# Kernel optimization log

Hardware: AMD Instinct MI355X
Metric: run time of the kernel (lower is better)

## Reference

```python
import jax, jax.numpy as jnp
import numpy as np

N_NODES = 65536   # sli * node = 512 * 128
N_EDGES = 524288  # avg degree 8
SLI, NODE = 512, 128
SLOPE = 0.01      # nn.LeakyReLU default negative_slope


def leaky_relu(v):
    return jnp.where(v >= 0, v, SLOPE * v)


def graph_conv(h, src, dst, W, b):
    """DGL GraphConv with norm='both': D_in^{-1/2} A D_out^{-1/2} h W + b, then LeakyReLU."""
    ones = jnp.ones(src.shape[0], dtype=h.dtype)
    out_deg = jnp.clip(jax.ops.segment_sum(ones, src, num_segments=N_NODES), 1.0)
    in_deg = jnp.clip(jax.ops.segment_sum(ones, dst, num_segments=N_NODES), 1.0)
    h = h * jax.lax.rsqrt(out_deg)[:, None]                     # src-side norm
    agg = jax.ops.segment_sum(h[src], dst, num_segments=N_NODES)  # gather + scatter-add
    agg = agg * jax.lax.rsqrt(in_deg)[:, None]                  # dst-side norm
    return leaky_relu(agg @ W + b)


def graphsage(x, src, dst, W, b):
    # x: [sli, C, node] -> [sli*node, C] -> GraphConv -> [sli, F, node]
    sli, C, node = x.shape
    h = x.transpose(0, 2, 1).reshape(-1, C)
    h = graph_conv(h, src, dst, W, b)
    return h.reshape(sli, node, -1).transpose(0, 2, 1)


def conv1x1(x, W, b):
    # pointwise Conv1d: x [S, Cin, N], W [Cout, Cin] -> [S, Cout, N]
    return jnp.einsum('scn,oc->son', x, W) + b[None, :, None]


def setup_inputs() -> dict:
    key = jax.random.key(0)
    ks = jax.random.split(key, 16)
    d = {
        'x': jax.random.normal(ks[0], (SLI, 128, NODE), dtype=jnp.float32),
        'edge_src': jax.random.randint(ks[1], (N_EDGES,), 0, N_NODES, dtype=jnp.int32),
        'edge_dst': jax.random.randint(ks[2], (N_EDGES,), 0, N_NODES, dtype=jnp.int32),
        'W_head': jax.random.normal(ks[3], (128, 128), dtype=jnp.float32) * 0.05,
        'b_head': jnp.zeros((128,), dtype=jnp.float32),
        'W_res0': jax.random.normal(ks[4], (128, 128), dtype=jnp.float32) * 0.05,
        'b_res0': jnp.zeros((128,), dtype=jnp.float32),
        'W_res1': jax.random.normal(ks[5], (128, 128), dtype=jnp.float32) * 0.05,
        'b_res1': jnp.zeros((128,), dtype=jnp.float32),
        'W_res2': jax.random.normal(ks[6], (128, 128), dtype=jnp.float32) * 0.05,
        'b_res2': jnp.zeros((128,), dtype=jnp.float32),
        'W_fusion': jax.random.normal(ks[7], (256, 512), dtype=jnp.float32) * 0.05,
        'b_fusion': jnp.zeros((256,), dtype=jnp.float32),
        'W_p1': jax.random.normal(ks[8], (256, 768), dtype=jnp.float32) * 0.05,
        'b_p1': jnp.zeros((256,), dtype=jnp.float32),
        'W_p2': jax.random.normal(ks[9], (64, 256), dtype=jnp.float32) * 0.05,
        'b_p2': jnp.zeros((64,), dtype=jnp.float32),
        'W_p3': jax.random.normal(ks[10], (2, 64), dtype=jnp.float32) * 0.05,
        'b_p3': jnp.zeros((2,), dtype=jnp.float32),
    }
    return d


def reference(x, edge_src, edge_dst, W_head, b_head, W_res0, b_res0, W_res1, b_res1,
              W_res2, b_res2, W_fusion, b_fusion, W_p1, b_p1, W_p2, b_p2, W_p3, b_p3):
    h = graphsage(x, edge_src, edge_dst, W_head, b_head)   # [S, 128, N]
    states = [h]
    for W, b in ((W_res0, b_res0), (W_res1, b_res1), (W_res2, b_res2)):
        h = graphsage(h, edge_src, edge_dst, W, b) + h     # residual
        states.append(h)
    state = jnp.concatenate(states, axis=1)                # [S, 512, N]
    fused = conv1x1(state, W_fusion, b_fusion)             # [S, 256, N]
    global_state = jnp.max(fused, axis=2, keepdims=True)   # [S, 256, 1]
    global_state = jnp.broadcast_to(global_state, (state.shape[0], 256, state.shape[2]))
    state = jnp.concatenate([global_state, state], axis=1) # [S, 768, N]
    y = leaky_relu(conv1x1(state, W_p1, b_p1))
    y = leaky_relu(conv1x1(y, W_p2, b_p2))
    return conv1x1(y, W_p3, b_p3)                          # [S, 2, N]
```

## Files before the change

kernel.cpp:

```cpp
#include <hip/hip_runtime.h>

#define NN 65536
#define NE 524288
#define SLOPE 0.01f

typedef unsigned short us;
typedef __attribute__((ext_vector_type(8))) short short8;
typedef __attribute__((ext_vector_type(4))) float f32x4;

__device__ __forceinline__ float leaky(float v) { return v >= 0.f ? v : SLOPE * v; }
__device__ __forceinline__ float b2f(us u) { return __uint_as_float(((unsigned)u) << 16); }
__device__ __forceinline__ us f2b(float f) {
  unsigned u = __float_as_uint(f);
  u += 0x7fffu + ((u >> 16) & 1u);
  return (us)(u >> 16);
}
__device__ __forceinline__ void split2(float v, us& hi, us& lo) {
  hi = f2b(v);
  lo = f2b(v - b2f(hi));
}

__device__ __forceinline__ void gload16(const void* g, void* l) {
  __builtin_amdgcn_global_load_lds(
      (const __attribute__((address_space(1))) unsigned int*)g,
      (__attribute__((address_space(3))) unsigned int*)l, 16, 0, 0);
}

__global__ void zero_ints(int* __restrict__ p, int n) {
  int i = blockIdx.x * blockDim.x + threadIdx.x;
  if (i < n) p[i] = 0;
}

__global__ void deg_count(const int* __restrict__ src, const int* __restrict__ dst,
                          int* __restrict__ cout, int* __restrict__ cin) {
  int e = blockIdx.x * blockDim.x + threadIdx.x;
  if (e < NE) {
    atomicAdd(&cout[src[e]], 1);
    atomicAdd(&cin[dst[e]], 1);
  }
}

__global__ void rs_kernel(const int* __restrict__ cout, const int* __restrict__ cin,
                          float* __restrict__ rs_out, float* __restrict__ rs_in) {
  int n = blockIdx.x * blockDim.x + threadIdx.x;
  if (n < NN) {
    rs_out[n] = rsqrtf((float)(cout[n] > 0 ? cout[n] : 1));
    rs_in[n]  = rsqrtf((float)(cin[n]  > 0 ? cin[n]  : 1));
  }
}

__global__ __launch_bounds__(1024) void scan_kernel(const int* __restrict__ cnt,
                                                    int* __restrict__ row_ptr) {
  __shared__ int part[1024];
  int t = threadIdx.x;
  int base = t * 64;
  int s = 0;
  for (int i = 0; i < 64; ++i) s += cnt[base + i];
  part[t] = s;
  __syncthreads();
  for (int d = 1; d < 1024; d <<= 1) {
    int v = (t >= d) ? part[t - d] : 0;
    __syncthreads();
    part[t] += v;
    __syncthreads();
  }
  int run = part[t] - s;
  for (int i = 0; i < 64; ++i) { row_ptr[base + i] = run; run += cnt[base + i]; }
  if (t == 1023) row_ptr[NN] = run;
}

__global__ void csr_fill(const int* __restrict__ src, const int* __restrict__ dst,
                         const int* __restrict__ row_ptr, int* __restrict__ cursor,
                         int* __restrict__ csr) {
  int e = blockIdx.x * blockDim.x + threadIdx.x;
  if (e < NE) {
    int d = dst[e];
    int pos = atomicAdd(&cursor[d], 1);
    csr[row_ptr[d] + pos] = src[e];
  }
}

__global__ __launch_bounds__(256) void transpose_x(const float* __restrict__ x,
                                                   us* __restrict__ h0h,
                                                   us* __restrict__ h0l) {
  __shared__ float tile[128][68];
  int s  = blockIdx.x >> 1;
  int vh = (blockIdx.x & 1) * 64;
  const float* xs = x + (size_t)s * 16384;
  int t = threadIdx.x;
  int v4 = t & 15, c0 = t >> 4;
  for (int p = 0; p < 8; ++p) {
    int c = c0 + p * 16;
    float4 val = *(const float4*)(xs + (size_t)c * 128 + vh + v4 * 4);
    *(float4*)&tile[c][v4 * 4] = val;
  }
  __syncthreads();
  int c4 = t & 31, v0 = t >> 5;
  for (int p = 0; p < 8; ++p) {
    int v = v0 + p * 8;
    float o[4];
    o[0] = tile[c4 * 4 + 0][v];
    o[1] = tile[c4 * 4 + 1][v];
    o[2] = tile[c4 * 4 + 2][v];
    o[3] = tile[c4 * 4 + 3][v];
    us hh[4], ll[4];
#pragma unroll
    for (int j = 0; j < 4; ++j) split2(o[j], hh[j], ll[j]);
    size_t off = (size_t)(s * 128 + vh + v) * 128 + c4 * 4;
    uint2 wh = make_uint2((unsigned)hh[0] | ((unsigned)hh[1] << 16),
                          (unsigned)hh[2] | ((unsigned)hh[3] << 16));
    uint2 wl = make_uint2((unsigned)ll[0] | ((unsigned)ll[1] << 16),
                          (unsigned)ll[2] | ((unsigned)ll[3] << 16));
    *(uint2*)(h0h + off) = wh;
    *(uint2*)(h0l + off) = wl;
  }
}

__global__ void wsplit(const float* __restrict__ src, us* __restrict__ bh,
                       us* __restrict__ bl, int N, int K, int ld, int koff) {
  int idx = blockIdx.x * 256 + threadIdx.x;
  if (idx >= N * K) return;
  int n = idx / K, k = idx - n * K;
  float v = src[(size_t)n * ld + koff + k];
  us hi, lo; split2(v, hi, lo);
  bh[idx] = hi; bl[idx] = lo;
}

__global__ void wsplit_t(const float* __restrict__ src, us* __restrict__ bh,
                         us* __restrict__ bl, int N, int K, int ld) {
  int idx = blockIdx.x * 256 + threadIdx.x;
  if (idx >= N * K) return;
  int n = idx / K, k = idx - n * K;
  float v = src[(size_t)k * ld + n];
  us hi, lo; split2(v, hi, lo);
  bh[idx] = hi; bl[idx] = lo;
}

__global__ __launch_bounds__(256) void aggregate(
    const us* __restrict__ hh, const us* __restrict__ hl, int lda,
    const int* __restrict__ row_ptr, const int* __restrict__ csr,
    const float* __restrict__ rs_out, const float* __restrict__ rs_in,
    us* __restrict__ aggh, us* __restrict__ aggl) {
  const int lane = threadIdx.x & 63;
  const int n = blockIdx.x * 4 + (threadIdx.x >> 6);
  const us* base = ((lane < 32) ? hh : hl) + (size_t)(lane & 31) * 4;
  const int b = row_ptr[n], e = row_ptr[n + 1];
  float a0 = 0.f, a1 = 0.f, a2 = 0.f, a3 = 0.f;
  int i = b;
  for (; i + 4 <= e; i += 4) {
    int s0 = csr[i], s1 = csr[i + 1], s2 = csr[i + 2], s3 = csr[i + 3];
    uint2 v0 = *(const uint2*)(base + (size_t)s0 * lda);
    uint2 v1 = *(const uint2*)(base + (size_t)s1 * lda);
    uint2 v2 = *(const uint2*)(base + (size_t)s2 * lda);
    uint2 v3 = *(const uint2*)(base + (size_t)s3 * lda);
    float w0 = rs_out[s0], w1 = rs_out[s1], w2 = rs_out[s2], w3 = rs_out[s3];
    a0 = fmaf(w0, __uint_as_float(v0.x << 16), a0);
    a1 = fmaf(w0, __uint_as_float(v0.x & 0xffff0000u), a1);
    a2 = fmaf(w0, __uint_as_float(v0.y << 16), a2);
    a3 = fmaf(w0, __uint_as_float(v0.y & 0xffff0000u), a3);
    a0 = fmaf(w1, __uint_as_float(v1.x << 16), a0);
    a1 = fmaf(w1, __uint_as_float(v1.x & 0xffff0000u), a1);
    a2 = fmaf(w1, __uint_as_float(v1.y << 16), a2);
    a3 = fmaf(w1, __uint_as_float(v1.y & 0xffff0000u), a3);
    a0 = fmaf(w2, __uint_as_float(v2.x << 16), a0);
    a1 = fmaf(w2, __uint_as_float(v2.x & 0xffff0000u), a1);
    a2 = fmaf(w2, __uint_as_float(v2.y << 16), a2);
    a3 = fmaf(w2, __uint_as_float(v2.y & 0xffff0000u), a3);
    a0 = fmaf(w3, __uint_as_float(v3.x << 16), a0);
    a1 = fmaf(w3, __uint_as_float(v3.x & 0xffff0000u), a1);
    a2 = fmaf(w3, __uint_as_float(v3.y << 16), a2);
    a3 = fmaf(w3, __uint_as_float(v3.y & 0xffff0000u), a3);
  }
  for (; i < e; ++i) {
    int s0 = csr[i];
    uint2 v0 = *(const uint2*)(base + (size_t)s0 * lda);
    float w0 = rs_out[s0];
    a0 = fmaf(w0, __uint_as_float(v0.x << 16), a0);
    a1 = fmaf(w0, __uint_as_float(v0.x & 0xffff0000u), a1);
    a2 = fmaf(w0, __uint_as_float(v0.y << 16), a2);
    a3 = fmaf(w0, __uint_as_float(v0.y & 0xffff0000u), a3);
  }
  a0 += __shfl_xor(a0, 32);
  a1 += __shfl_xor(a1, 32);
  a2 += __shfl_xor(a2, 32);
  a3 += __shfl_xor(a3, 32);
  const float ri = rs_in[n];
  a0 *= ri; a1 *= ri; a2 *= ri; a3 *= ri;
  us h[4], l[4];
  split2(a0, h[0], l[0]); split2(a1, h[1], l[1]);
  split2(a2, h[2], l[2]); split2(a3, h[3], l[3]);
  size_t o = (size_t)n * 128 + (size_t)(lane & 31) * 4;
  if (lane < 32) {
    uint2 wv = make_uint2((unsigned)h[0] | ((unsigned)h[1] << 16),
                          (unsigned)h[2] | ((unsigned)h[3] << 16));
    *(uint2*)(aggh + o) = wv;
  } else {
    uint2 wv = make_uint2((unsigned)l[0] | ((unsigned)l[1] << 16),
                          (unsigned)l[2] | ((unsigned)l[3] << 16));
    *(uint2*)(aggl + o) = wv;
  }
}

template<int KTOT, int NF, int MODE, int NSPLIT>
__global__ __launch_bounds__(512, 4) void mgemm(
    const us* __restrict__ Ah, const us* __restrict__ Al, int lda,
    const us* __restrict__ Bh, const us* __restrict__ Bl,
    const float* __restrict__ bias,
    float* __restrict__ outf, us* __restrict__ outh, us* __restrict__ outl,
    int ldo, int colOff,
    const us* __restrict__ prevh, const us* __restrict__ prevl,
    const float* __restrict__ gcon) {
  constexpr int BN  = NF * 64;
  constexpr int LB  = (NF == 2) ? 7 : 6;
  constexpr int NT  = KTOT / 32;
  constexpr int LPT = 2 + (BN * 8) / 512;

  __shared__ __align__(16) us sAh[2][4][128][8];
  __shared__ __align__(16) us sAl[2][4][128][8];
  __shared__ __align__(16) us sBh[2][4][BN][8];
  __shared__ __align__(16) us sBl[2][4][BN][8];

  const int t = threadIdx.x;
  int mb, nb;
  if constexpr (NSPLIT == 2) {
    int lid = (blockIdx.x & 7) * ((int)gridDim.x >> 3) + (blockIdx.x >> 3);
    mb = lid >> 1; nb = lid & 1;
  } else {
    mb = blockIdx.x; nb = 0;
  }
  const int mbase = mb * 128;
  const int nbase = nb * BN;

  const us* gp[LPT];
  us* lp0[LPT];
  us* lp1[LPT];
#pragma unroll
  for (int i = 0; i < LPT; ++i) {
    int id = i * 512 + t;
    if (id < 512) {
      int row = id & 127, kb = id >> 7;
      gp[i]  = Ah + (size_t)(mbase + row) * lda + kb * 8;
      lp0[i] = &sAh[0][kb][row][0];
      lp1[i] = &sAh[1][kb][row][0];
    } else if (id < 1024) {
      int c = id - 512;
      int row = c & 127, kb = c >> 7;
      gp[i]  = Al + (size_t)(mbase + row) * lda + kb * 8;
      lp0[i] = &sAl[0][kb][row][0];
      lp1[i] = &sAl[1][kb][row][0];
    } else if (id < 1024 + BN * 4) {
      int c = id - 1024;
      int row = c & (BN - 1), kb = c >> LB;
      gp[i]  = Bh + (size_t)(nbase + row) * KTOT + kb * 8;
      lp0[i] = &sBh[0][kb][row][0];
      lp1[i] = &sBh[1][kb][row][0];
    } else {
      int c = id - 1024 - BN * 4;
      int row = c & (BN - 1), kb = c >> LB;
      gp[i]  = Bl + (size_t)(nbase + row) * KTOT + kb * 8;
      lp0[i] = &sBl[0][kb][row][0];
      lp1[i] = &sBl[1][kb][row][0];
    }
  }

  const int lane = t & 63, wvi = t >> 6;
  const int wm = wvi & 1, wn = wvi >> 1;
  const int l15 = lane & 15, lkb = lane >> 4;

  f32x4 acc[4][NF];
#pragma unroll
  for (int i = 0; i < 4; ++i)
#pragma unroll
    for (int j = 0; j < NF; ++j)
#pragma unroll
      for (int e = 0; e < 4; ++e) acc[i][j][e] = 0.f;

  auto stageb = [&](us* const* lp, int k0) {
#pragma unroll
    for (int i = 0; i < LPT; ++i) gload16(gp[i] + k0, lp[i]);
  };
  auto waitL = [&]() {
    if constexpr (LPT == 4) asm volatile("s_waitcnt vmcnt(4)" ::: "memory");
    else                    asm volatile("s_waitcnt vmcnt(3)" ::: "memory");
    __builtin_amdgcn_sched_barrier(0);
  };
  auto wait0 = [&]() {
    asm volatile("s_waitcnt vmcnt(0)" ::: "memory");
    __builtin_amdgcn_sched_barrier(0);
  };
  auto bar = [&]() {
    __builtin_amdgcn_s_barrier();
    __builtin_amdgcn_sched_barrier(0);
  };
  auto kstep = [&](us (&bAh)[4][128][8], us (&bAl)[4][128][8],
                   us (&bBh)[4][BN][8], us (&bBl)[4][BN][8]) {
    short8 ah[4], al[4], bh[NF], bl[NF];
#pragma unroll
    for (int fm = 0; fm < 4; ++fm) {
      ah[fm] = *(const short8*)&bAh[lkb][wm * 64 + fm * 16 + l15][0];
      al[fm] = *(const short8*)&bAl[lkb][wm * 64 + fm * 16 + l15][0];
    }
#pragma unroll
    for (int fn = 0; fn < NF; ++fn) {
      bh[fn] = *(const short8*)&bBh[lkb][wn * (NF * 16) + fn * 16 + l15][0];
      bl[fn] = *(const short8*)&bBl[lkb][wn * (NF * 16) + fn * 16 + l15][0];
    }
    __builtin_amdgcn_s_setprio(1);
#pragma unroll
    for (int fm = 0; fm < 4; ++fm)
#pragma unroll
      for (int fn = 0; fn < NF; ++fn)
        acc[fm][fn] = __builtin_amdgcn_mfma_f32_16x16x32_bf16(ah[fm], bh[fn], acc[fm][fn], 0, 0, 0);
#pragma unroll
    for (int fm = 0; fm < 4; ++fm)
#pragma unroll
      for (int fn = 0; fn < NF; ++fn)
        acc[fm][fn] = __builtin_amdgcn_mfma_f32_16x16x32_bf16(al[fm], bh[fn], acc[fm][fn], 0, 0, 0);
#pragma unroll
    for (int fm = 0; fm < 4; ++fm)
#pragma unroll
      for (int fn = 0; fn < NF; ++fn)
        acc[fm][fn] = __builtin_amdgcn_mfma_f32_16x16x32_bf16(ah[fm], bl[fn], acc[fm][fn], 0, 0, 0);
    __builtin_amdgcn_s_setprio(0);
  };

  stageb(lp0, 0);
  stageb(lp1, 32);
#pragma unroll 1
  for (int kt = 0; kt < NT; kt += 2) {
    waitL(); bar();
    kstep(sAh[0], sAl[0], sBh[0], sBl[0]);
    bar();
    if (kt + 2 < NT) stageb(lp0, (kt + 2) * 32);
    if (kt + 3 < NT) waitL(); else wait0();
    bar();
    kstep(sAh[1], sAl[1], sBh[1], sBl[1]);
    bar();
    if (kt + 3 < NT) stageb(lp1, (kt + 3) * 32);
  }

  if constexpr (MODE == 0 || MODE == 1 || MODE == 3) {
    const float* gc = (MODE == 3) ? (gcon + (size_t)mb * 256 + nbase) : nullptr;
#pragma unroll
    for (int fm = 0; fm < 4; ++fm)
#pragma unroll
      for (int fn = 0; fn < NF; ++fn) {
        const int col = wn * (NF * 16) + fn * 16 + l15;
        float bb = bias[nbase + col];
        if constexpr (MODE == 3) bb += gc[col];
#pragma unroll
        for (int r = 0; r < 4; ++r) {
          const int row = mbase + wm * 64 + fm * 16 + lkb * 4 + r;
          float v = leaky(acc[fm][fn][r] + bb);
          const size_t off = (size_t)row * ldo + colOff + nbase + col;
          if constexpr (MODE == 1) v += b2f(prevh[off - 128]) + b2f(prevl[off - 128]);
          us hi, lo; split2(v, hi, lo);
          outh[off] = hi;
          outl[off] = lo;
        }
      }
  } else if constexpr (MODE == 2) {
    __shared__ float red[2][128];
#pragma unroll
    for (int fn = 0; fn < NF; ++fn) {
      float m = acc[0][fn][0];
#pragma unroll
      for (int fm = 0; fm < 4; ++fm)
#pragma unroll
        for (int r = 0; r < 4; ++r) m = fmaxf(m, acc[fm][fn][r]);
      m = fmaxf(m, __shfl_xor(m, 16));
      m = fmaxf(m, __shfl_xor(m, 32));
      if (lane < 16) red[wm][wn * (NF * 16) + fn * 16 + l15] = m;
    }
    __syncthreads();
    if (t < 128)
      outf[(size_t)mb * 256 + nbase + t] = fmaxf(red[0][t], red[1][t]) + bias[nbase + t];
  } else {
#pragma unroll
    for (int fm = 0; fm < 4; ++fm) {
      const int col = wn * 16 + l15;
      const float bb = bias[col];
#pragma unroll
      for (int r = 0; r < 4; ++r) {
        const int row = mbase + wm * 64 + fm * 16 + lkb * 4 + r;
        outf[(size_t)row * 64 + col] = leaky(acc[fm][0][r] + bb);
      }
    }
  }
}

__global__ void gcon_kernel(const float* __restrict__ gmax, const float* __restrict__ Wp1,
                            float* __restrict__ gcon) {
  __shared__ float g[256];
  int s = blockIdx.x, o = threadIdx.x;
  g[o] = gmax[(size_t)s * 256 + o];
  __syncthreads();
  float acc = 0.f;
  const float* wr = Wp1 + (size_t)o * 768;
#pragma unroll 8
  for (int c = 0; c < 256; ++c) acc += g[c] * wr[c];
  gcon[(size_t)s * 256 + o] = acc;
}

__global__ void p3_kernel(const float* __restrict__ y2, const float* __restrict__ W,
                          const float* __restrict__ b, float* __restrict__ out) {
  __shared__ float w0[64], w1[64];
  int t = threadIdx.x;
  if (t < 64) { w0[t] = W[t]; w1[t] = W[64 + t]; }
  __syncthreads();
  int n = blockIdx.x * 256 + t;
  const float* row = y2 + (size_t)n * 64;
  float a0 = b[0], a1 = b[1];
#pragma unroll
  for (int j = 0; j < 64; j += 4) {
    float4 v = *(const float4*)(row + j);
    a0 += v.x * w0[j] + v.y * w0[j + 1] + v.z * w0[j + 2] + v.w * w0[j + 3];
    a1 += v.x * w1[j] + v.y * w1[j + 1] + v.z * w1[j + 2] + v.w * w1[j + 3];
  }
  int s = n >> 7, vv = n & 127;
  out[((size_t)s * 2 + 0) * 128 + vv] = a0;
  out[((size_t)s * 2 + 1) * 128 + vv] = a1;
}

extern "C" void kernel_launch(void* const* d_in, const int* in_sizes, int n_in,
                              void* d_out, int out_size, void* d_ws, size_t ws_size,
                              hipStream_t stream) {
  const float* x        = (const float*)d_in[0];
  const int*   esrc     = (const int*)d_in[1];
  const int*   edst     = (const int*)d_in[2];
  const float* W_head   = (const float*)d_in[3];
  const float* b_head   = (const float*)d_in[4];
  const float* W_res[3] = {(const float*)d_in[5], (const float*)d_in[7], (const float*)d_in[9]};
  const float* b_res[3] = {(const float*)d_in[6], (const float*)d_in[8], (const float*)d_in[10]};
  const float* W_fusion = (const float*)d_in[11];
  const float* b_fusion = (const float*)d_in[12];
  const float* W_p1     = (const float*)d_in[13];
  const float* b_p1     = (const float*)d_in[14];
  const float* W_p2     = (const float*)d_in[15];
  const float* b_p2     = (const float*)d_in[16];
  const float* W_p3     = (const float*)d_in[17];
  const float* b_p3     = (const float*)d_in[18];
  float* outp = (float*)d_out;

  char* w = (char*)d_ws;
  size_t off = 0;
  auto alloc = [&](size_t bytes) { char* p = w + off; off += (bytes + 255) & ~(size_t)255; return p; };

  us* states_h = (us*)alloc((size_t)NN * 512 * 2);
  us* states_l = (us*)alloc((size_t)NN * 512 * 2);
  char* regionA = alloc((size_t)NN * 128 * 2 * 4);
  us* h0h  = (us*)regionA;
  us* h0l  = (us*)(regionA + (size_t)NN * 128 * 2);
  us* aggh = (us*)(regionA + (size_t)NN * 128 * 4);
  us* aggl = (us*)(regionA + (size_t)NN * 128 * 6);
  us* y1h  = (us*)regionA;
  us* y1l  = (us*)(regionA + (size_t)NN * 256 * 2);
  float* y2 = (float*)states_h;

  float* gmax   = (float*)alloc(512 * 256 * 4);
  float* gcon   = (float*)alloc(512 * 256 * 4);
  float* rs_out = (float*)alloc((size_t)NN * 4);
  float* rs_in  = (float*)alloc((size_t)NN * 4);
  us* cWh[4]; us* cWl[4];
  for (int l = 0; l < 4; ++l) { cWh[l] = (us*)alloc(128 * 128 * 2); cWl[l] = (us*)alloc(128 * 128 * 2); }
  us* fWh  = (us*)alloc(256 * 512 * 2);
  us* fWl  = (us*)alloc(256 * 512 * 2);
  us* p1Wh = (us*)alloc(256 * 512 * 2);
  us* p1Wl = (us*)alloc(256 * 512 * 2);
  us* p2Wh = (us*)alloc(64 * 256 * 2);
  us* p2Wl = (us*)alloc(64 * 256 * 2);
  int* cnt_out = (int*)alloc((size_t)NN * 4);
  int* cnt_in  = (int*)alloc((size_t)NN * 4);
  int* cursor  = (int*)alloc((size_t)NN * 4);
  int* row_ptr = (int*)alloc(((size_t)NN + 1) * 4);
  int* csr     = (int*)alloc((size_t)NE * 4);

  zero_ints<<<(3 * NN + 255) / 256, 256, 0, stream>>>(cnt_out, 3 * NN);
  deg_count<<<NE / 256, 256, 0, stream>>>(esrc, edst, cnt_out, cnt_in);
  rs_kernel<<<NN / 256, 256, 0, stream>>>(cnt_out, cnt_in, rs_out, rs_in);
  scan_kernel<<<1, 1024, 0, stream>>>(cnt_in, row_ptr);
  csr_fill<<<NE / 256, 256, 0, stream>>>(esrc, edst, row_ptr, cursor, csr);

  transpose_x<<<1024, 256, 0, stream>>>(x, h0h, h0l);
  const float* cW[4] = {W_head, W_res[0], W_res[1], W_res[2]};
  for (int l = 0; l < 4; ++l)
    wsplit_t<<<64, 256, 0, stream>>>(cW[l], cWh[l], cWl[l], 128, 128, 128);
  wsplit<<<512, 256, 0, stream>>>(W_fusion, fWh, fWl, 256, 512, 512, 0);
  wsplit<<<512, 256, 0, stream>>>(W_p1, p1Wh, p1Wl, 256, 512, 768, 256);
  wsplit<<<64, 256, 0, stream>>>(W_p2, p2Wh, p2Wl, 64, 256, 256, 0);

  const float* cB[4] = {b_head, b_res[0], b_res[1], b_res[2]};
  aggregate<<<NN / 4, 256, 0, stream>>>(h0h, h0l, 128, row_ptr, csr, rs_out, rs_in, aggh, aggl);
  mgemm<128, 2, 0, 1><<<512, 512, 0, stream>>>(aggh, aggl, 128, cWh[0], cWl[0], cB[0],
                                               nullptr, states_h, states_l, 512, 0,
                                               nullptr, nullptr, nullptr);
  for (int l = 1; l <= 3; ++l) {
    aggregate<<<NN / 4, 256, 0, stream>>>(states_h + (size_t)(l - 1) * 128,
                                          states_l + (size_t)(l - 1) * 128, 512,
                                          row_ptr, csr, rs_out, rs_in, aggh, aggl);
    mgemm<128, 2, 1, 1><<<512, 512, 0, stream>>>(aggh, aggl, 128, cWh[l], cWl[l], cB[l],
                                                 nullptr, states_h, states_l, 512, l * 128,
                                                 states_h, states_l, nullptr);
  }
  mgemm<512, 2, 2, 2><<<1024, 512, 0, stream>>>(states_h, states_l, 512, fWh, fWl, b_fusion,
                                                gmax, nullptr, nullptr, 0, 0,
                                                nullptr, nullptr, nullptr);
  gcon_kernel<<<512, 256, 0, stream>>>(gmax, W_p1, gcon);
  mgemm<512, 2, 3, 2><<<1024, 512, 0, stream>>>(states_h, states_l, 512, p1Wh, p1Wl, b_p1,
                                                nullptr, y1h, y1l, 256, 0,
                                                nullptr, nullptr, gcon);
  mgemm<256, 1, 4, 1><<<512, 512, 0, stream>>>(y1h, y1l, 256, p2Wh, p2Wl, b_p2,
                                               y2, nullptr, nullptr, 0, 0,
                                               nullptr, nullptr, nullptr);
  p3_kernel<<<NN / 256, 256, 0, stream>>>(y2, W_p3, b_p3, outp);
}
```

Baseline: 628.4 us.

## Replace GEMM kernel with 256-row tiles covering full N per block

Rewrites the split-bf16 MFMA GEMM to process 256 rows per block and the full output width (up to 256 columns) in one block, with a flat LDS buffer and phased fragment loads separated by barriers. This removes the N-split and the cross-block max reduction, and reduces redundant reloading of A tiles across column blocks. In exchange, LDS use and register pressure per block grow and there are fewer blocks (256) than CUs on some launches, which may reduce occupancy and latency hiding.

```diff
diff --git a/kernel.cpp b/kernel.cpp
--- a/kernel.cpp
+++ b/kernel.cpp
@@ -201,8 +201,8 @@
   }
 }
 
-template<int KTOT, int NF, int MODE, int NSPLIT>
-__global__ __launch_bounds__(512, 4) void mgemm(
+template<int KTOT, int BN, int WM, int PH, int MODE>
+__global__ __launch_bounds__(512) void mgemm8(
     const us* __restrict__ Ah, const us* __restrict__ Al, int lda,
     const us* __restrict__ Bh, const us* __restrict__ Bl,
     const float* __restrict__ bias,
@@ -210,149 +210,134 @@
     int ldo, int colOff,
     const us* __restrict__ prevh, const us* __restrict__ prevl,
     const float* __restrict__ gcon) {
-  constexpr int BN  = NF * 64;
-  constexpr int LB  = (NF == 2) ? 7 : 6;
+  constexpr int WN  = 8 / WM;
+  constexpr int FM  = 16 / WM;
+  constexpr int FMP = FM / PH;
   constexpr int NT  = KTOT / 32;
-  constexpr int LPT = 2 + (BN * 8) / 512;
-
-  __shared__ __align__(16) us sAh[2][4][128][8];
-  __shared__ __align__(16) us sAl[2][4][128][8];
-  __shared__ __align__(16) us sBh[2][4][BN][8];
-  __shared__ __align__(16) us sBl[2][4][BN][8];
+  constexpr int LBN = (BN == 256) ? 8 : ((BN == 128) ? 7 : 6);
+  constexpr int CHT = 2048 + BN * 8;
+  constexpr int LPT = CHT / 512;
+
+  __shared__ __align__(16) us L[2][CHT * 8];
 
   const int t = threadIdx.x;
-  int mb, nb;
-  if constexpr (NSPLIT == 2) {
-    int lid = (blockIdx.x & 7) * ((int)gridDim.x >> 3) + (blockIdx.x >> 3);
-    mb = lid >> 1; nb = lid & 1;
-  } else {
-    mb = blockIdx.x; nb = 0;
-  }
-  const int mbase = mb * 128;
-  const int nbase = nb * BN;
+  const int mbase = blockIdx.x * 256;
 
   const us* gp[LPT];
-  us* lp0[LPT];
-  us* lp1[LPT];
 #pragma unroll
   for (int i = 0; i < LPT; ++i) {
     int id = i * 512 + t;
-    if (id < 512) {
-      int row = id & 127, kb = id >> 7;
-      gp[i]  = Ah + (size_t)(mbase + row) * lda + kb * 8;
-      lp0[i] = &sAh[0][kb][row][0];
-      lp1[i] = &sAh[1][kb][row][0];
-    } else if (id < 1024) {
-      int c = id - 512;
-      int row = c & 127, kb = c >> 7;
-      gp[i]  = Al + (size_t)(mbase + row) * lda + kb * 8;
-      lp0[i] = &sAl[0][kb][row][0];
-      lp1[i] = &sAl[1][kb][row][0];
-    } else if (id < 1024 + BN * 4) {
-      int c = id - 1024;
-      int row = c & (BN - 1), kb = c >> LB;
-      gp[i]  = Bh + (size_t)(nbase + row) * KTOT + kb * 8;
-      lp0[i] = &sBh[0][kb][row][0];
-      lp1[i] = &sBh[1][kb][row][0];
+    if (id < 1024) {
+      int row = id & 255, kb = id >> 8;
+      gp[i] = Ah + (size_t)(mbase + row) * lda + kb * 8;
+    } else if (id < 2048) {
+      int c = id - 1024, row = c & 255, kb = c >> 8;
+      gp[i] = Al + (size_t)(mbase + row) * lda + kb * 8;
+    } else if (id < 2048 + BN * 4) {
+      int c = id - 2048, row = c & (BN - 1), kb = c >> LBN;
+      gp[i] = Bh + (size_t)row * KTOT + kb * 8;
     } else {
-      int c = id - 1024 - BN * 4;
-      int row = c & (BN - 1), kb = c >> LB;
-      gp[i]  = Bl + (size_t)(nbase + row) * KTOT + kb * 8;
-      lp0[i] = &sBl[0][kb][row][0];
-      lp1[i] = &sBl[1][kb][row][0];
+      int c = id - 2048 - BN * 4, row = c & (BN - 1), kb = c >> LBN;
+      gp[i] = Bl + (size_t)row * KTOT + kb * 8;
     }
   }
 
   const int lane = t & 63, wvi = t >> 6;
-  const int wm = wvi & 1, wn = wvi >> 1;
+  const int wm = wvi & (WM - 1), wn = wvi / WM;
   const int l15 = lane & 15, lkb = lane >> 4;
-
-  f32x4 acc[4][NF];
-#pragma unroll
-  for (int i = 0; i < 4; ++i)
-#pragma unroll
-    for (int j = 0; j < NF; ++j)
+  const int wrow = wm * (256 / WM);
+
+  f32x4 acc[FM][4];
+#pragma unroll
+  for (int i = 0; i < FM; ++i)
+#pragma unroll
+    for (int j = 0; j < 4; ++j)
 #pragma unroll
       for (int e = 0; e < 4; ++e) acc[i][j][e] = 0.f;
 
-  auto stageb = [&](us* const* lp, int k0) {
-#pragma unroll
-    for (int i = 0; i < LPT; ++i) gload16(gp[i] + k0, lp[i]);
+  auto stage = [&](us* Lb, int k0) {
+#pragma unroll
+    for (int i = 0; i < LPT; ++i)
+      gload16(gp[i] + k0, Lb + (size_t)(i * 512 + t) * 8);
   };
   auto waitL = [&]() {
-    if constexpr (LPT == 4) asm volatile("s_waitcnt vmcnt(4)" ::: "memory");
-    else                    asm volatile("s_waitcnt vmcnt(3)" ::: "memory");
+    if constexpr (LPT == 8)      asm volatile("s_waitcnt vmcnt(8)" ::: "memory");
+    else if constexpr (LPT == 6) asm volatile("s_waitcnt vmcnt(6)" ::: "memory");
+    else                         asm volatile("s_waitcnt vmcnt(5)" ::: "memory");
     __builtin_amdgcn_sched_barrier(0);
   };
   auto wait0 = [&]() {
     asm volatile("s_waitcnt vmcnt(0)" ::: "memory");
     __builtin_amdgcn_sched_barrier(0);
   };
-  auto bar = [&]() {
-    __builtin_amdgcn_s_barrier();
-    __builtin_amdgcn_sched_barrier(0);
+  auto phases = [&](const us* Lb) {
+#pragma unroll
+    for (int p = 0; p < PH; ++p) {
+      short8 ah[FMP], al[FMP], bh[4], bl[4];
+#pragma unroll
+      for (int f = 0; f < FMP; ++f) {
+        const int arow = wrow + (p * FMP + f) * 16 + l15;
+        ah[f] = *(const short8*)(Lb + ((size_t)(lkb * 256 + arow)) * 8);
+        al[f] = *(const short8*)(Lb + ((size_t)(1024 + lkb * 256 + arow)) * 8);
+      }
+#pragma unroll
+      for (int fn = 0; fn < 4; ++fn) {
+        const int bcol = wn * 64 + fn * 16 + l15;
+        bh[fn] = *(const short8*)(Lb + ((size_t)(2048 + lkb * BN + bcol)) * 8);
+        bl[fn] = *(const short8*)(Lb + ((size_t)(2048 + BN * 4 + lkb * BN + bcol)) * 8);
+      }
+      __builtin_amdgcn_s_setprio(1);
+#pragma unroll
+      for (int f = 0; f < FMP; ++f)
+#pragma unroll
+        for (int fn = 0; fn < 4; ++fn)
+          acc[p * FMP + f][fn] =
+              __builtin_amdgcn_mfma_f32_16x16x32_bf16(ah[f], bh[fn], acc[p * FMP + f][fn], 0, 0, 0);
+#pragma unroll
+      for (int f = 0; f < FMP; ++f)
+#pragma unroll
+        for (int fn = 0; fn < 4; ++fn)
+          acc[p * FMP + f][fn] =
+              __builtin_amdgcn_mfma_f32_16x16x32_bf16(al[f], bh[fn], acc[p * FMP + f][fn], 0, 0, 0);
+#pragma unroll
+      for (int f = 0; f < FMP; ++f)
+#pragma unroll
+        for (int fn = 0; fn < 4; ++fn)
+          acc[p * FMP + f][fn] =
+              __builtin_amdgcn_mfma_f32_16x16x32_bf16(ah[f], bl[fn], acc[p * FMP + f][fn], 0, 0, 0);
+      __builtin_amdgcn_s_setprio(0);
+      __builtin_amdgcn_s_barrier();
+    }
   };
-  auto kstep = [&](us (&bAh)[4][128][8], us (&bAl)[4][128][8],
-                   us (&bBh)[4][BN][8], us (&bBl)[4][BN][8]) {
-    short8 ah[4], al[4], bh[NF], bl[NF];
-#pragma unroll
-    for (int fm = 0; fm < 4; ++fm) {
-      ah[fm] = *(const short8*)&bAh[lkb][wm * 64 + fm * 16 + l15][0];
-      al[fm] = *(const short8*)&bAl[lkb][wm * 64 + fm * 16 + l15][0];
-    }
-#pragma unroll
-    for (int fn = 0; fn < NF; ++fn) {
-      bh[fn] = *(const short8*)&bBh[lkb][wn * (NF * 16) + fn * 16 + l15][0];
-      bl[fn] = *(const short8*)&bBl[lkb][wn * (NF * 16) + fn * 16 + l15][0];
-    }
-    __builtin_amdgcn_s_setprio(1);
-#pragma unroll
-    for (int fm = 0; fm < 4; ++fm)
-#pragma unroll
-      for (int fn = 0; fn < NF; ++fn)
-        acc[fm][fn] = __builtin_amdgcn_mfma_f32_16x16x32_bf16(ah[fm], bh[fn], acc[fm][fn], 0, 0, 0);
-#pragma unroll
-    for (int fm = 0; fm < 4; ++fm)
-#pragma unroll
-      for (int fn = 0; fn < NF; ++fn)
-        acc[fm][fn] = __builtin_amdgcn_mfma_f32_16x16x32_bf16(al[fm], bh[fn], acc[fm][fn], 0, 0, 0);
-#pragma unroll
-    for (int fm = 0; fm < 4; ++fm)
-#pragma unroll
-      for (int fn = 0; fn < NF; ++fn)
-        acc[fm][fn] = __builtin_amdgcn_mfma_f32_16x16x32_bf16(ah[fm], bl[fn], acc[fm][fn], 0, 0, 0);
-    __builtin_amdgcn_s_setprio(0);
-  };
-
-  stageb(lp0, 0);
-  stageb(lp1, 32);
+
+  stage(L[0], 0);
+  if (NT > 1) stage(L[1], 32);
 #pragma unroll 1
   for (int kt = 0; kt < NT; kt += 2) {
-    waitL(); bar();
-    kstep(sAh[0], sAl[0], sBh[0], sBl[0]);
-    bar();
-    if (kt + 2 < NT) stageb(lp0, (kt + 2) * 32);
+    waitL();
+    __builtin_amdgcn_s_barrier();
+    phases(L[0]);
+    if (kt + 2 < NT) stage(L[0], (kt + 2) * 32);
     if (kt + 3 < NT) waitL(); else wait0();
-    bar();
-    kstep(sAh[1], sAl[1], sBh[1], sBl[1]);
-    bar();
-    if (kt + 3 < NT) stageb(lp1, (kt + 3) * 32);
+    __builtin_amdgcn_s_barrier();
+    phases(L[1]);
+    if (kt + 3 < NT) stage(L[1], (kt + 3) * 32);
   }
 
   if constexpr (MODE == 0 || MODE == 1 || MODE == 3) {
-    const float* gc = (MODE == 3) ? (gcon + (size_t)mb * 256 + nbase) : nullptr;
-#pragma unroll
-    for (int fm = 0; fm < 4; ++fm)
-#pragma unroll
-      for (int fn = 0; fn < NF; ++fn) {
-        const int col = wn * (NF * 16) + fn * 16 + l15;
-        float bb = bias[nbase + col];
+    const float* gc = (MODE == 3) ? (gcon + (size_t)(blockIdx.x * 2 + wm) * 256) : nullptr;
+#pragma unroll
+    for (int fm = 0; fm < FM; ++fm)
+#pragma unroll
+      for (int fn = 0; fn < 4; ++fn) {
+        const int col = wn * 64 + fn * 16 + l15;
+        float bb = bias[col];
         if constexpr (MODE == 3) bb += gc[col];
 #pragma unroll
         for (int r = 0; r < 4; ++r) {
-          const int row = mbase + wm * 64 + fm * 16 + lkb * 4 + r;
+          const int row = mbase + wrow + fm * 16 + lkb * 4 + r;
           float v = leaky(acc[fm][fn][r] + bb);
-          const size_t off = (size_t)row * ldo + colOff + nbase + col;
+          const size_t off = (size_t)row * ldo + colOff + col;
           if constexpr (MODE == 1) v += b2f(prevh[off - 128]) + b2f(prevl[off - 128]);
           us hi, lo; split2(v, hi, lo);
           outh[off] = hi;
@@ -360,32 +345,33 @@
         }
       }
   } else if constexpr (MODE == 2) {
-    __shared__ float red[2][128];
-#pragma unroll
-    for (int fn = 0; fn < NF; ++fn) {
+#pragma unroll
+    for (int fn = 0; fn < 4; ++fn) {
       float m = acc[0][fn][0];
 #pragma unroll
-      for (int fm = 0; fm < 4; ++fm)
+      for (int fm = 0; fm < FM; ++fm)
 #pragma unroll
         for (int r = 0; r < 4; ++r) m = fmaxf(m, acc[fm][fn][r]);
       m = fmaxf(m, __shfl_xor(m, 16));
       m = fmaxf(m, __shfl_xor(m, 32));
-      if (lane < 16) red[wm][wn * (NF * 16) + fn * 16 + l15] = m;
-    }
-    __syncthreads();
-    if (t < 128)
-      outf[(size_t)mb * 256 + nbase + t] = fmaxf(red[0][t], red[1][t]) + bias[nbase + t];
-  } else {
-#pragma unroll
-    for (int fm = 0; fm < 4; ++fm) {
-      const int col = wn * 16 + l15;
-      const float bb = bias[col];
-#pragma unroll
-      for (int r = 0; r < 4; ++r) {
-        const int row = mbase + wm * 64 + fm * 16 + lkb * 4 + r;
-        outf[(size_t)row * 64 + col] = leaky(acc[fm][0][r] + bb);
+      if (lane < 16) {
+        const int col = wn * 64 + fn * 16 + l15;
+        outf[(size_t)(blockIdx.x * 2 + wm) * 256 + col] = m + bias[col];
       }
     }
+  } else {
+#pragma unroll
+    for (int fm = 0; fm < FM; ++fm)
+#pragma unroll
+      for (int fn = 0; fn < 4; ++fn) {
+        const int col = fn * 16 + l15;
+        const float bb = bias[col];
+#pragma unroll
+        for (int r = 0; r < 4; ++r) {
+          const int row = mbase + wrow + fm * 16 + lkb * 4 + r;
+          outf[(size_t)row * 64 + col] = leaky(acc[fm][fn][r] + bb);
+        }
+      }
   }
 }
 
@@ -491,26 +477,26 @@
 
   const float* cB[4] = {b_head, b_res[0], b_res[1], b_res[2]};
   aggregate<<<NN / 4, 256, 0, stream>>>(h0h, h0l, 128, row_ptr, csr, rs_out, rs_in, aggh, aggl);
-  mgemm<128, 2, 0, 1><<<512, 512, 0, stream>>>(aggh, aggl, 128, cWh[0], cWl[0], cB[0],
-                                               nullptr, states_h, states_l, 512, 0,
-                                               nullptr, nullptr, nullptr);
+  mgemm8<128, 128, 4, 2, 0><<<256, 512, 0, stream>>>(aggh, aggl, 128, cWh[0], cWl[0], cB[0],
+                                                     nullptr, states_h, states_l, 512, 0,
+                                                     nullptr, nullptr, nullptr);
   for (int l = 1; l <= 3; ++l) {
     aggregate<<<NN / 4, 256, 0, stream>>>(states_h + (size_t)(l - 1) * 128,
                                           states_l + (size_t)(l - 1) * 128, 512,
                                           row_ptr, csr, rs_out, rs_in, aggh, aggl);
-    mgemm<128, 2, 1, 1><<<512, 512, 0, stream>>>(aggh, aggl, 128, cWh[l], cWl[l], cB[l],
-                                                 nullptr, states_h, states_l, 512, l * 128,
-                                                 states_h, states_l, nullptr);
-  }
-  mgemm<512, 2, 2, 2><<<1024, 512, 0, stream>>>(states_h, states_l, 512, fWh, fWl, b_fusion,
-                                                gmax, nullptr, nullptr, 0, 0,
-                                                nullptr, nullptr, nullptr);
+    mgemm8<128, 128, 4, 2, 1><<<256, 512, 0, stream>>>(aggh, aggl, 128, cWh[l], cWl[l], cB[l],
+                                                       nullptr, states_h, states_l, 512, l * 128,
+                                                       states_h, states_l, nullptr);
+  }
+  mgemm8<512, 256, 2, 4, 2><<<256, 512, 0, stream>>>(states_h, states_l, 512, fWh, fWl, b_fusion,
+                                                     gmax, nullptr, nullptr, 0, 0,
+                                                     nullptr, nullptr, nullptr);
   gcon_kernel<<<512, 256, 0, stream>>>(gmax, W_p1, gcon);
-  mgemm<512, 2, 3, 2><<<1024, 512, 0, stream>>>(states_h, states_l, 512, p1Wh, p1Wl, b_p1,
-                                                nullptr, y1h, y1l, 256, 0,
-                                                nullptr, nullptr, gcon);
-  mgemm<256, 1, 4, 1><<<512, 512, 0, stream>>>(y1h, y1l, 256, p2Wh, p2Wl, b_p2,
-                                               y2, nullptr, nullptr, 0, 0,
-                                               nullptr, nullptr, nullptr);
+  mgemm8<512, 256, 2, 4, 3><<<256, 512, 0, stream>>>(states_h, states_l, 512, p1Wh, p1Wl, b_p1,
+                                                     nullptr, y1h, y1l, 256, 0,
+                                                     nullptr, nullptr, gcon);
+  mgemm8<256, 64, 8, 2, 4><<<256, 512, 0, stream>>>(y1h, y1l, 256, p2Wh, p2Wl, b_p2,
+                                                    y2, nullptr, nullptr, 0, 0,
+                                                    nullptr, nullptr, nullptr);
   p3_kernel<<<NN / 256, 256, 0, stream>>>(y2, W_p3, b_p3, outp);
 }
```

After: 616.5 us. Within noise of the previous version (-1.9%).
